# Performance work log

Hardware: AMD Instinct MI355X
Metric: run time of the kernel (lower is better)

## Reference

```python
import jax, jax.numpy as jnp
import numpy as np

NUM_HEADS = 12
EPS = 1e-6


def setup_inputs() -> dict:
    key = jax.random.key(0)
    k1, k2, k3, k4 = jax.random.split(key, 4)
    N, B, D = 1025, 8, 768
    x = jax.random.normal(k1, (N, B, D), dtype=jnp.float32)
    # torch nn.Linear weights: [out_features, in_features]
    w_qkv = jax.random.normal(k2, (3 * D, D), dtype=jnp.float32) * (D ** -0.5)
    w_proj = jax.random.normal(k3, (D, D), dtype=jnp.float32) * (D ** -0.5)
    b_proj = jax.random.normal(k4, (D,), dtype=jnp.float32) * 0.01
    return {"x": x, "w_qkv": w_qkv, "w_proj": w_proj, "b_proj": b_proj}


def reference(x, w_qkv, w_proj, b_proj):
    N, B, D = x.shape
    H = NUM_HEADS
    hd = D // H
    scale = hd ** -0.5
    scale_vv = scale * 1.0  # scale_multiplier = 1.0

    xb = jnp.transpose(x, (1, 0, 2))  # [B, N, D]
    qkv = xb @ w_qkv.T  # [B, N, 3D]
    qkv = qkv.reshape(B, N, 3, H, hd).transpose(2, 0, 3, 1, 4)  # [3, B, H, N, hd]
    q, k, v = qkv[0], qkv[1], qkv[2]

    # QK path: only row 0 of out_ori survives the masking, compute just that row
    scores0 = jnp.einsum('bhqd,bhkd->bhqk', q[:, :, :1], k) * scale  # [B,H,1,N]
    attn0 = jax.nn.softmax(scores0, axis=-1)
    out0 = jnp.einsum('bhqk,bhkd->bhqd', attn0, v)  # [B,H,1,hd]

    # VV cosine path: only rows 1: survive
    vn = v / jnp.maximum(jnp.linalg.norm(v, axis=-1, keepdims=True), EPS)
    scores_vv = jnp.einsum('bhqd,bhkd->bhqk', vn[:, :, 1:], vn) * scale_vv  # [B,H,N-1,N]
    attn_vv = jax.nn.softmax(scores_vv, axis=-1)
    out_vv = jnp.einsum('bhqk,bhkd->bhqd', attn_vv, v)  # [B,H,N-1,hd]

    out = jnp.concatenate([out0, out_vv], axis=2)  # [B,H,N,hd]
    out = out.transpose(0, 2, 1, 3).reshape(B, N, D)
    out = out @ w_proj.T + b_proj
    return jnp.transpose(out, (1, 0, 2))  # [N, B, D]
```

## Files before the change

### kernel.cpp

```cpp
#include <hip/hip_runtime.h>

typedef unsigned short u16;
typedef unsigned int   u32;
typedef __attribute__((ext_vector_type(8))) short short8;
typedef __attribute__((ext_vector_type(4))) float f32x4;

#define AS1 __attribute__((address_space(1)))
#define AS3 __attribute__((address_space(3)))

#define NSEQ  1025
#define BB    8
#define DD    768
#define HH    12
#define MROWS 8200
#define MPAD  8320
#define KPAD  1088

__device__ __forceinline__ void gl2lds16(const void* g, void* l) {
  __builtin_amdgcn_global_load_lds((const AS1 u32*)g, (AS3 u32*)l, 16, 0, 0);
}
__device__ __forceinline__ u16 f2bf(float f) {
  u32 u = __float_as_uint(f);
  return (u16)((u + 0x7FFFu + ((u >> 16) & 1u)) >> 16);
}
__device__ __forceinline__ float bf2f(u16 u) { return __uint_as_float(((u32)u) << 16); }

__global__ __launch_bounds__(256) void prep(const float* __restrict__ x,
                                            const float* __restrict__ wqkv,
                                            const float* __restrict__ wproj,
                                            u16* __restrict__ xb,
                                            u16* __restrict__ wkv,
                                            u16* __restrict__ wpj,
                                            float* __restrict__ q0) {
  __shared__ float red[256];
  const int XB_G  = MPAD * 192;
  const int WKV_G = 1536 * 192;
  const int WPJ_G = 768 * 192;
  int tid = threadIdx.x;
  if (blockIdx.x >= 7968) {
    int bid = blockIdx.x - 7968;
    int b = bid / HH, c = bid - b * HH;
    int dp = (c << 6) + (tid >> 2), part = tid & 3;
    const float4* x4 = (const float4*)(x + (size_t)b * DD + part * 192);
    const float4* w4 = (const float4*)(wqkv + (size_t)dp * DD + part * 192);
    float acc = 0.f;
#pragma unroll 4
    for (int e = 0; e < 48; ++e) {
      float4 a = x4[e], w = w4[e];
      acc += a.x * w.x + a.y * w.y + a.z * w.z + a.w * w.w;
    }
    red[tid] = acc;
    __syncthreads();
    if (part == 0) q0[b * DD + dp] = red[tid] + red[tid + 1] + red[tid + 2] + red[tid + 3];
    return;
  }
  int g = blockIdx.x * 256 + tid;
  float4 v;
  u16* dst;
  size_t di;
  if (g < XB_G) {
    int m = g / 192, e4 = g - m * 192;
    if (m < MROWS) {
      int bb = m / NSEQ, ns = m - bb * NSEQ;
      v = ((const float4*)x)[(size_t)(ns * BB + bb) * 192 + e4];
    } else {
      v.x = v.y = v.z = v.w = 0.f;
    }
    dst = xb; di = (size_t)g;
  } else if (g < XB_G + WKV_G) {
    int r = g - XB_G;
    v = ((const float4*)wqkv)[(size_t)147456 + r];
    dst = wkv; di = (size_t)r;
  } else {
    int r = g - XB_G - WKV_G;
    v = ((const float4*)wproj)[r];
    dst = wpj; di = (size_t)r;
  }
  uint2 o;
  o.x = (u32)f2bf(v.x) | ((u32)f2bf(v.y) << 16);
  o.y = (u32)f2bf(v.z) | ((u32)f2bf(v.w) << 16);
  ((uint2*)dst)[di] = o;
}

template <int MODE, int NT>
__global__ __launch_bounds__(256) void gemm_bt(const u16* __restrict__ A,
                                               const u16* __restrict__ W,
                                               u16* __restrict__ Cbf,
                                               float* __restrict__ Cf,
                                               const float* __restrict__ bias,
                                               int ldc) {
  __shared__ u16 sA[128 * 64];
  __shared__ u16 sW[128 * 64];
  const int id = blockIdx.x;
  const int rx = id & 7, qx = id >> 3;
  const int kq = qx / NT;
  const int m_t = rx + (kq << 3);
  if (m_t > 64) return;
  const int n_t = qx - kq * NT;
  const int m0 = m_t << 7, n0 = n_t << 7;

  const int tid = threadIdx.x;
  const int w = tid >> 6, lane = tid & 63;
  const int wm = w & 1, wn = w >> 1;
  const int lc = lane & 15, lr = lane >> 4;

  f32x4 zero4 = {0.f, 0.f, 0.f, 0.f};
  f32x4 acc[4][4];
#pragma unroll
  for (int i = 0; i < 4; ++i)
#pragma unroll
    for (int j = 0; j < 4; ++j) acc[i][j] = zero4;

  const int r0 = tid >> 3;
  const int ko = (tid & 7) << 3;
  const u16* gA = A + (size_t)(m0 + r0) * DD + ko;
  const u16* gW = W + (size_t)(n0 + r0) * DD + ko;
  char* lA = (char*)sA + tid * 16;
  char* lW = (char*)sW + tid * 16;

#pragma unroll 1
  for (int kt = 0; kt < 12; ++kt) {
    __syncthreads();
#pragma unroll
    for (int j = 0; j < 4; ++j) {
      gl2lds16(gA + (size_t)j * 32 * DD + kt * 64, lA + j * 4096);
      gl2lds16(gW + (size_t)j * 32 * DD + kt * 64, lW + j * 4096);
    }
    __syncthreads();
#pragma unroll
    for (int kk = 0; kk < 2; ++kk) {
      short8 af[4], wf[4];
#pragma unroll
      for (int mt = 0; mt < 4; ++mt)
        af[mt] = *(const short8*)((char*)sA + ((wm << 6) + (mt << 4) + lc) * 128 + (kk << 6) + (lr << 4));
#pragma unroll
      for (int nt = 0; nt < 4; ++nt)
        wf[nt] = *(const short8*)((char*)sW + ((wn << 6) + (nt << 4) + lc) * 128 + (kk << 6) + (lr << 4));
#pragma unroll
      for (int mt = 0; mt < 4; ++mt)
#pragma unroll
        for (int nt = 0; nt < 4; ++nt)
          acc[mt][nt] = __builtin_amdgcn_mfma_f32_16x16x32_bf16(af[mt], wf[nt], acc[mt][nt], 0, 0, 0);
    }
  }

  if (MODE == 0) {
#pragma unroll
    for (int mt = 0; mt < 4; ++mt)
#pragma unroll
      for (int r = 0; r < 4; ++r) {
        int m = m0 + (wm << 6) + (mt << 4) + (lr << 2) + r;
        if (m < MROWS) {
          size_t base = (size_t)m * ldc + n0 + (wn << 6) + lc;
#pragma unroll
          for (int nt = 0; nt < 4; ++nt) Cbf[base + (nt << 4)] = f2bf(acc[mt][nt][r]);
        }
      }
  } else {
    float b4[4];
#pragma unroll
    for (int nt = 0; nt < 4; ++nt) b4[nt] = bias[n0 + (wn << 6) + (nt << 4) + lc];
#pragma unroll
    for (int mt = 0; mt < 4; ++mt)
#pragma unroll
      for (int r = 0; r < 4; ++r) {
        int m = m0 + (wm << 6) + (mt << 4) + (lr << 2) + r;
        if (m < MROWS) {
          int bb = m / NSEQ;
          int ns = m - bb * NSEQ;
          float* o = Cf + (size_t)ns * (BB * DD) + bb * DD + n0 + (wn << 6) + lc;
#pragma unroll
          for (int nt = 0; nt < 4; ++nt) o[nt << 4] = acc[mt][nt][r] + b4[nt];
        }
      }
  }
}

__global__ __launch_bounds__(256) void transpose_v(const u16* __restrict__ kv,
                                                   u16* __restrict__ vT,
                                                   u16* __restrict__ vn) {
  __shared__ u16 tile[64][72];
  __shared__ float red[256];
  __shared__ float sInv[64];
  int bid = blockIdx.x;
  int kc = bid % 17;
  int t2 = bid / 17;
  int h = t2 % HH, b = t2 / HH;
  int tid = threadIdx.x;
  int kl = tid >> 2, dc = (tid & 3) << 4;
  int key = kc * 64 + kl;
  u32 vals[8];
  if (key < NSEQ) {
    const u32* g = (const u32*)(kv + ((size_t)b * NSEQ + key) * 1536 + DD + h * 64 + dc);
#pragma unroll
    for (int i = 0; i < 8; ++i) vals[i] = g[i];
  } else {
#pragma unroll
    for (int i = 0; i < 8; ++i) vals[i] = 0;
  }
  float part = 0.f;
#pragma unroll
  for (int i = 0; i < 8; ++i) {
    float a = bf2f((u16)(vals[i] & 0xFFFF));
    float c = bf2f((u16)(vals[i] >> 16));
    part += a * a + c * c;
    ((u32*)&tile[kl][dc])[i] = vals[i];
  }
  red[tid] = part;
  __syncthreads();
  if ((tid & 3) == 0) {
    float s = red[tid] + red[tid + 1] + red[tid + 2] + red[tid + 3];
    sInv[kl] = (key < NSEQ) ? 1.0f / fmaxf(sqrtf(s), 1e-6f) : 0.0f;
  }
  __syncthreads();
  float iv = sInv[kl];
  u32 ovn[8];
#pragma unroll
  for (int i = 0; i < 8; ++i) {
    float a = bf2f((u16)(vals[i] & 0xFFFF)) * iv;
    float c = bf2f((u16)(vals[i] >> 16)) * iv;
    ovn[i] = (u32)f2bf(a) | ((u32)f2bf(c) << 16);
  }
  u32* on = (u32*)(vn + ((size_t)(b * HH + h) * KPAD + key) * 64 + dc);
#pragma unroll
  for (int i = 0; i < 8; ++i) on[i] = ovn[i];
  int dl = tid >> 2, ks = (tid & 3) << 4;
  u32 ov[8];
#pragma unroll
  for (int i = 0; i < 8; ++i)
    ov[i] = (u32)tile[ks + 2 * i][dl] | ((u32)tile[ks + 2 * i + 1][dl] << 16);
  u16* o = vT + (size_t)(b * HH + h) * 64 * KPAD + (size_t)dl * KPAD + kc * 64 + ks;
#pragma unroll
  for (int i = 0; i < 8; ++i) ((u32*)o)[i] = ov[i];
}

__global__ __launch_bounds__(256) void vv_attn(const u16* __restrict__ vn,
                                               const u16* __restrict__ vT,
                                               u16* __restrict__ attn,
                                               const float* __restrict__ q0,
                                               const u16* __restrict__ kv) {
  __shared__ __align__(16) char smem[51200];
  const int tid = threadIdx.x;
  const int bh = blockIdx.x;
  const int b = bh / HH, h = bh - b * HH;

  if (blockIdx.y == 8) {
    float* sq  = (float*)smem;
    float* sc  = (float*)(smem + 256);
    float* red = (float*)(smem + 4608);
    float (*rpv)[68] = (float(*)[68])(smem + 5632);
    if (tid < 64) sq[tid] = q0[b * DD + h * 64 + tid];
    __syncthreads();
    float mx = -1e30f;
    for (int n = tid; n < NSEQ; n += 256) {
      const u32* kr = (const u32*)(kv + ((size_t)b * NSEQ + n) * 1536 + h * 64);
      float s = 0.f;
#pragma unroll
      for (int i = 0; i < 32; ++i) {
        u32 u = kr[i];
        s += bf2f((u16)(u & 0xFFFF)) * sq[2 * i] + bf2f((u16)(u >> 16)) * sq[2 * i + 1];
      }
      s *= 0.125f;
      sc[n] = s;
      mx = fmaxf(mx, s);
    }
    red[tid] = mx;
    __syncthreads();
    for (int st = 128; st > 0; st >>= 1) {
      if (tid < st) red[tid] = fmaxf(red[tid], red[tid + st]);
      __syncthreads();
    }
    mx = red[0];
    __syncthreads();
    float ds = 0.f;
    for (int n = tid; n < NSEQ; n += 256) {
      float p = __expf(sc[n] - mx);
      sc[n] = p;
      ds += p;
    }
    red[tid] = ds;
    __syncthreads();
    for (int st = 128; st > 0; st >>= 1) {
      if (tid < st) red[tid] += red[tid + st];
      __syncthreads();
    }
    float den = red[0];
    __syncthreads();
    int kp = tid >> 3, dc = (tid & 7) << 3;
    const u16* vb = kv + (size_t)b * NSEQ * 1536 + DD + h * 64 + dc;
    float acc[8];
#pragma unroll
    for (int i = 0; i < 8; ++i) acc[i] = 0.f;
#pragma unroll 4
    for (int j = 0; j < 32; ++j) {
      int n = kp + (j << 5);
      uint4 v = *(const uint4*)(vb + (size_t)n * 1536);
      float p = sc[n];
      acc[0] += p * bf2f((u16)(v.x & 0xFFFF));
      acc[1] += p * bf2f((u16)(v.x >> 16));
      acc[2] += p * bf2f((u16)(v.y & 0xFFFF));
      acc[3] += p * bf2f((u16)(v.y >> 16));
      acc[4] += p * bf2f((u16)(v.z & 0xFFFF));
      acc[5] += p * bf2f((u16)(v.z >> 16));
      acc[6] += p * bf2f((u16)(v.w & 0xFFFF));
      acc[7] += p * bf2f((u16)(v.w >> 16));
    }
    if (kp == 0) {
      uint4 v = *(const uint4*)(vb + (size_t)1024 * 1536);
      float p = sc[1024];
      acc[0] += p * bf2f((u16)(v.x & 0xFFFF));
      acc[1] += p * bf2f((u16)(v.x >> 16));
      acc[2] += p * bf2f((u16)(v.y & 0xFFFF));
      acc[3] += p * bf2f((u16)(v.y >> 16));
      acc[4] += p * bf2f((u16)(v.z & 0xFFFF));
      acc[5] += p * bf2f((u16)(v.z >> 16));
      acc[6] += p * bf2f((u16)(v.w & 0xFFFF));
      acc[7] += p * bf2f((u16)(v.w >> 16));
    }
#pragma unroll
    for (int i = 0; i < 8; ++i) rpv[kp][dc + i] = acc[i];
    __syncthreads();
    if (tid < 64) {
      float s = 0.f;
#pragma unroll
      for (int p = 0; p < 32; ++p) s += rpv[p][tid];
      attn[(size_t)b * NSEQ * DD + h * 64 + tid] = f2bf(s / den);
    }
    return;
  }

  char* cQ = smem;
  char* cK = smem + 16384;
  char* cV = smem + 24576;
  char* cP = smem + 32768;

  const int w = tid >> 6, lane = tid & 63;
  const int lc = lane & 15, lr = lane >> 4;
  const int m0 = blockIdx.y << 7;
  const char* nb = (const char*)(vn + (size_t)bh * KPAD * 64);
  const char* tb = (const char*)(vT + (size_t)bh * 64 * KPAD);

#pragma unroll
  for (int j = 0; j < 4; ++j) {
    int lin = (w << 12) + (j << 10) + (lane << 4);
    int hf = lin >> 13, r = (lin >> 6) & 127, off = lin & 63;
    gl2lds16(nb + (size_t)(1 + m0 + r) * 128 + hf * 64 + off, cQ + lin);
  }

  f32x4 zero4 = {0.f, 0.f, 0.f, 0.f};
  f32x4 oacc[2][4];
  f32x4 dacc[2];
#pragma unroll
  for (int i = 0; i < 2; ++i) {
    dacc[i] = zero4;
#pragma unroll
    for (int j = 0; j < 4; ++j) oacc[i][j] = zero4;
  }
  short8 ones;
#pragma unroll
  for (int i = 0; i < 8; ++i) ones[i] = (short)0x3F80;

#pragma unroll 1
  for (int kt = 0; kt < 17; ++kt) {
    __syncthreads();
#pragma unroll
    for (int j = 0; j < 2; ++j) {
      int lin = (w << 11) + (j << 10) + (lane << 4);
      int hf = lin >> 12, r = (lin >> 6) & 63, off = lin & 63;
      gl2lds16(nb + (size_t)(kt * 64 + r) * 128 + hf * 64 + off, cK + lin);
      gl2lds16(tb + (size_t)r * (KPAD * 2) + kt * 128 + hf * 64 + off, cV + lin);
    }
    __syncthreads();

    f32x4 sacc[4][2];
#pragma unroll
    for (int mt = 0; mt < 4; ++mt)
#pragma unroll
      for (int nt = 0; nt < 2; ++nt) sacc[mt][nt] = zero4;
#pragma unroll
    for (int kk = 0; kk < 2; ++kk) {
      short8 ak[4], bq[2];
#pragma unroll
      for (int mt = 0; mt < 4; ++mt)
        ak[mt] = *(const short8*)(cK + (kk << 12) + ((mt << 4) + lc) * 64 + (lr << 4));
#pragma unroll
      for (int nt = 0; nt < 2; ++nt)
        bq[nt] = *(const short8*)(cQ + (kk << 13) + ((w << 5) + (nt << 4) + lc) * 64 + (lr << 4));
#pragma unroll
      for (int mt = 0; mt < 4; ++mt)
#pragma unroll
        for (int nt = 0; nt < 2; ++nt)
          sacc[mt][nt] = __builtin_amdgcn_mfma_f32_16x16x32_bf16(ak[mt], bq[nt], sacc[mt][nt], 0, 0, 0);
    }

#pragma unroll
    for (int mt = 0; mt < 4; ++mt) {
      int kl0 = (mt << 4) + (lr << 2);
#pragma unroll
      for (int nt = 0; nt < 2; ++nt) {
        int q = (w << 5) + (nt << 4) + lc;
        float c0 = sacc[mt][nt][0], c1 = sacc[mt][nt][1];
        float c2 = sacc[mt][nt][2], c3 = sacc[mt][nt][3];
        float p0 = __builtin_fmaf(c0, __builtin_fmaf(c0, 0.0078125f, 0.125f), 1.0f);
        float p1 = __builtin_fmaf(c1, __builtin_fmaf(c1, 0.0078125f, 0.125f), 1.0f);
        float p2 = __builtin_fmaf(c2, __builtin_fmaf(c2, 0.0078125f, 0.125f), 1.0f);
        float p3 = __builtin_fmaf(c3, __builtin_fmaf(c3, 0.0078125f, 0.125f), 1.0f);
        uint2 pv;
        pv.x = __builtin_amdgcn_perm(__float_as_uint(p1), __float_as_uint(p0), 0x07060302u);
        pv.y = __builtin_amdgcn_perm(__float_as_uint(p3), __float_as_uint(p2), 0x07060302u);
        if (kt == 16) {
          pv.x = (kl0 == 0) ? (pv.x & 0xFFFFu) : 0u;
          pv.y = 0u;
        }
        *(uint2*)(cP + q * 144 + (kl0 << 1)) = pv;
      }
    }

#pragma unroll
    for (int kk = 0; kk < 2; ++kk) {
      short8 ap[2], bv[4];
#pragma unroll
      for (int mt = 0; mt < 2; ++mt)
        ap[mt] = *(const short8*)(cP + ((w << 5) + (mt << 4) + lc) * 144 + (kk << 6) + (lr << 4));
#pragma unroll
      for (int nt = 0; nt < 4; ++nt)
        bv[nt] = *(const short8*)(cV + (kk << 12) + ((nt << 4) + lc) * 64 + (lr << 4));
#pragma unroll
      for (int mt = 0; mt < 2; ++mt) {
#pragma unroll
        for (int nt = 0; nt < 4; ++nt)
          oacc[mt][nt] = __builtin_amdgcn_mfma_f32_16x16x32_bf16(ap[mt], bv[nt], oacc[mt][nt], 0, 0, 0);
        dacc[mt] = __builtin_amdgcn_mfma_f32_16x16x32_bf16(ap[mt], ones, dacc[mt], 0, 0, 0);
      }
    }
  }

#pragma unroll
  for (int mt = 0; mt < 2; ++mt) {
#pragma unroll
    for (int r = 0; r < 4; ++r) {
      int q = (w << 5) + (mt << 4) + (lr << 2) + r;
      int nseq = 1 + m0 + q;
      float rdn = 1.0f / dacc[mt][r];
      size_t obase = ((size_t)b * NSEQ + nseq) * DD + h * 64 + lc;
#pragma unroll
      for (int nt = 0; nt < 4; ++nt) attn[obase + (nt << 4)] = f2bf(oacc[mt][nt][r] * rdn);
    }
  }
}

extern "C" void kernel_launch(void* const* d_in, const int* in_sizes, int n_in,
                              void* d_out, int out_size, void* d_ws, size_t ws_size,
                              hipStream_t stream) {
  const float* x      = (const float*)d_in[0];
  const float* w_qkv  = (const float*)d_in[1];
  const float* w_proj = (const float*)d_in[2];
  const float* b_proj = (const float*)d_in[3];
  float* out = (float*)d_out;
  char* ws = (char*)d_ws;

  u16*   xb   = (u16*)(ws + 0);
  u16*   vT   = (u16*)(ws + 0);
  u16*   wkv  = (u16*)(ws + 13369344);
  u16*   wpj  = (u16*)(ws + 15728640);
  u16*   kvb  = (u16*)(ws + 16908288);
  float* q0   = (float*)(ws + 42467328);
  u16*   attn = (u16*)(ws + 42491904);
  u16*   vn   = (u16*)(ws + 55271424);

  prep<<<8064, 256, 0, stream>>>(x, w_qkv, w_proj, xb, wkv, wpj, q0);
  gemm_bt<0, 12><<<864, 256, 0, stream>>>(xb, wkv, kvb, nullptr, nullptr, 1536);
  transpose_v<<<1632, 256, 0, stream>>>(kvb, vT, vn);
  vv_attn<<<dim3(96, 9), 256, 0, stream>>>(vn, vT, attn, q0, kvb);
  gemm_bt<1, 6><<<432, 256, 0, stream>>>(attn, wpj, nullptr, out, b_proj, 768);
}
```

Baseline: 236.1 us.

## Split row-0 attention into own kernel and hold Q fragments in registers

The row-0 QK softmax path moves out of vv_attn into a separate row0_attn kernel, so vv_attn no longer carries its shared-memory footprint or branch. vv_attn now loads its Q tile into registers once and reuses the LDS space for P, which cuts LDS from 51200 to 33792 bytes. It also sets launch_bounds(256,4) for higher occupancy and shrinks the P row stride from 144 to 136 bytes. The trade-offs are one extra kernel launch, higher register pressure from the persistent Q fragments, and possible LDS bank-conflict changes from the new stride.

Result: slower. 251.3 us (+6.4%).

```diff
diff --git a/kernel.cpp b/kernel.cpp
--- a/kernel.cpp
+++ b/kernel.cpp
@@ -35,7 +35,6 @@
   __shared__ float red[256];
   const int XB_G  = MPAD * 192;
   const int WKV_G = 1536 * 192;
-  const int WPJ_G = 768 * 192;
   int tid = threadIdx.x;
   if (blockIdx.x >= 7968) {
     int bid = blockIdx.x - 7968;
@@ -234,109 +233,108 @@
   for (int i = 0; i < 8; ++i) ((u32*)o)[i] = ov[i];
 }
 
-__global__ __launch_bounds__(256) void vv_attn(const u16* __restrict__ vn,
-                                               const u16* __restrict__ vT,
-                                               u16* __restrict__ attn,
-                                               const float* __restrict__ q0,
-                                               const u16* __restrict__ kv) {
-  __shared__ __align__(16) char smem[51200];
-  const int tid = threadIdx.x;
+__global__ __launch_bounds__(256) void row0_attn(const float* __restrict__ q0,
+                                                 const u16* __restrict__ kv,
+                                                 u16* __restrict__ attn) {
+  __shared__ float sq[64];
+  __shared__ float sc[NSEQ];
+  __shared__ float red[256];
+  __shared__ float rpv[32][68];
+  int bid = blockIdx.x;
+  int b = bid / HH, h = bid - b * HH;
+  int tid = threadIdx.x;
+  if (tid < 64) sq[tid] = q0[b * DD + h * 64 + tid];
+  __syncthreads();
+  float mx = -1e30f;
+  for (int n = tid; n < NSEQ; n += 256) {
+    const u32* kr = (const u32*)(kv + ((size_t)b * NSEQ + n) * 1536 + h * 64);
+    float s = 0.f;
+#pragma unroll
+    for (int i = 0; i < 32; ++i) {
+      u32 u = kr[i];
+      s += bf2f((u16)(u & 0xFFFF)) * sq[2 * i] + bf2f((u16)(u >> 16)) * sq[2 * i + 1];
+    }
+    s *= 0.125f;
+    sc[n] = s;
+    mx = fmaxf(mx, s);
+  }
+  red[tid] = mx;
+  __syncthreads();
+  for (int st = 128; st > 0; st >>= 1) {
+    if (tid < st) red[tid] = fmaxf(red[tid], red[tid + st]);
+    __syncthreads();
+  }
+  mx = red[0];
+  __syncthreads();
+  float ds = 0.f;
+  for (int n = tid; n < NSEQ; n += 256) {
+    float p = __expf(sc[n] - mx);
+    sc[n] = p;
+    ds += p;
+  }
+  red[tid] = ds;
+  __syncthreads();
+  for (int st = 128; st > 0; st >>= 1) {
+    if (tid < st) red[tid] += red[tid + st];
+    __syncthreads();
+  }
+  float den = red[0];
+  __syncthreads();
+  int kp = tid >> 3, dc = (tid & 7) << 3;
+  const u16* vb = kv + (size_t)b * NSEQ * 1536 + DD + h * 64 + dc;
+  float acc[8];
+#pragma unroll
+  for (int i = 0; i < 8; ++i) acc[i] = 0.f;
+#pragma unroll 4
+  for (int j = 0; j < 32; ++j) {
+    int n = kp + (j << 5);
+    uint4 v = *(const uint4*)(vb + (size_t)n * 1536);
+    float p = sc[n];
+    acc[0] += p * bf2f((u16)(v.x & 0xFFFF));
+    acc[1] += p * bf2f((u16)(v.x >> 16));
+    acc[2] += p * bf2f((u16)(v.y & 0xFFFF));
+    acc[3] += p * bf2f((u16)(v.y >> 16));
+    acc[4] += p * bf2f((u16)(v.z & 0xFFFF));
+    acc[5] += p * bf2f((u16)(v.z >> 16));
+    acc[6] += p * bf2f((u16)(v.w & 0xFFFF));
+    acc[7] += p * bf2f((u16)(v.w >> 16));
+  }
+  if (kp == 0) {
+    uint4 v = *(const uint4*)(vb + (size_t)1024 * 1536);
+    float p = sc[1024];
+    acc[0] += p * bf2f((u16)(v.x & 0xFFFF));
+    acc[1] += p * bf2f((u16)(v.x >> 16));
+    acc[2] += p * bf2f((u16)(v.y & 0xFFFF));
+    acc[3] += p * bf2f((u16)(v.y >> 16));
+    acc[4] += p * bf2f((u16)(v.z & 0xFFFF));
+    acc[5] += p * bf2f((u16)(v.z >> 16));
+    acc[6] += p * bf2f((u16)(v.w & 0xFFFF));
+    acc[7] += p * bf2f((u16)(v.w >> 16));
+  }
+#pragma unroll
+  for (int i = 0; i < 8; ++i) rpv[kp][dc + i] = acc[i];
+  __syncthreads();
+  if (tid < 64) {
+    float s = 0.f;
+#pragma unroll
+    for (int p = 0; p < 32; ++p) s += rpv[p][tid];
+    attn[(size_t)b * NSEQ * DD + h * 64 + tid] = f2bf(s / den);
+  }
+}
+
+__global__ __launch_bounds__(256, 4) void vv_attn(const u16* __restrict__ vn,
+                                                  const u16* __restrict__ vT,
+                                                  u16* __restrict__ attn) {
+  __shared__ __align__(16) char smem[33792];
+  char* cP = smem;
+  char* cK = smem + 17408;
+  char* cV = smem + 25600;
+
+  const int tid = threadIdx.x, w = tid >> 6, lane = tid & 63;
+  const int lc = lane & 15, lr = lane >> 4;
   const int bh = blockIdx.x;
+  const int m0 = blockIdx.y << 7;
   const int b = bh / HH, h = bh - b * HH;
-
-  if (blockIdx.y == 8) {
-    float* sq  = (float*)smem;
-    float* sc  = (float*)(smem + 256);
-    float* red = (float*)(smem + 4608);
-    float (*rpv)[68] = (float(*)[68])(smem + 5632);
-    if (tid < 64) sq[tid] = q0[b * DD + h * 64 + tid];
-    __syncthreads();
-    float mx = -1e30f;
-    for (int n = tid; n < NSEQ; n += 256) {
-      const u32* kr = (const u32*)(kv + ((size_t)b * NSEQ + n) * 1536 + h * 64);
-      float s = 0.f;
-#pragma unroll
-      for (int i = 0; i < 32; ++i) {
-        u32 u = kr[i];
-        s += bf2f((u16)(u & 0xFFFF)) * sq[2 * i] + bf2f((u16)(u >> 16)) * sq[2 * i + 1];
-      }
-      s *= 0.125f;
-      sc[n] = s;
-      mx = fmaxf(mx, s);
-    }
-    red[tid] = mx;
-    __syncthreads();
-    for (int st = 128; st > 0; st >>= 1) {
-      if (tid < st) red[tid] = fmaxf(red[tid], red[tid + st]);
-      __syncthreads();
-    }
-    mx = red[0];
-    __syncthreads();
-    float ds = 0.f;
-    for (int n = tid; n < NSEQ; n += 256) {
-      float p = __expf(sc[n] - mx);
-      sc[n] = p;
-      ds += p;
-    }
-    red[tid] = ds;
-    __syncthreads();
-    for (int st = 128; st > 0; st >>= 1) {
-      if (tid < st) red[tid] += red[tid + st];
-      __syncthreads();
-    }
-    float den = red[0];
-    __syncthreads();
-    int kp = tid >> 3, dc = (tid & 7) << 3;
-    const u16* vb = kv + (size_t)b * NSEQ * 1536 + DD + h * 64 + dc;
-    float acc[8];
-#pragma unroll
-    for (int i = 0; i < 8; ++i) acc[i] = 0.f;
-#pragma unroll 4
-    for (int j = 0; j < 32; ++j) {
-      int n = kp + (j << 5);
-      uint4 v = *(const uint4*)(vb + (size_t)n * 1536);
-      float p = sc[n];
-      acc[0] += p * bf2f((u16)(v.x & 0xFFFF));
-      acc[1] += p * bf2f((u16)(v.x >> 16));
-      acc[2] += p * bf2f((u16)(v.y & 0xFFFF));
-      acc[3] += p * bf2f((u16)(v.y >> 16));
-      acc[4] += p * bf2f((u16)(v.z & 0xFFFF));
-      acc[5] += p * bf2f((u16)(v.z >> 16));
-      acc[6] += p * bf2f((u16)(v.w & 0xFFFF));
-      acc[7] += p * bf2f((u16)(v.w >> 16));
-    }
-    if (kp == 0) {
-      uint4 v = *(const uint4*)(vb + (size_t)1024 * 1536);
-      float p = sc[1024];
-      acc[0] += p * bf2f((u16)(v.x & 0xFFFF));
-      acc[1] += p * bf2f((u16)(v.x >> 16));
-      acc[2] += p * bf2f((u16)(v.y & 0xFFFF));
-      acc[3] += p * bf2f((u16)(v.y >> 16));
-      acc[4] += p * bf2f((u16)(v.z & 0xFFFF));
-      acc[5] += p * bf2f((u16)(v.z >> 16));
-      acc[6] += p * bf2f((u16)(v.w & 0xFFFF));
-      acc[7] += p * bf2f((u16)(v.w >> 16));
-    }
-#pragma unroll
-    for (int i = 0; i < 8; ++i) rpv[kp][dc + i] = acc[i];
-    __syncthreads();
-    if (tid < 64) {
-      float s = 0.f;
-#pragma unroll
-      for (int p = 0; p < 32; ++p) s += rpv[p][tid];
-      attn[(size_t)b * NSEQ * DD + h * 64 + tid] = f2bf(s / den);
-    }
-    return;
-  }
-
-  char* cQ = smem;
-  char* cK = smem + 16384;
-  char* cV = smem + 24576;
-  char* cP = smem + 32768;
-
-  const int w = tid >> 6, lane = tid & 63;
-  const int lc = lane & 15, lr = lane >> 4;
-  const int m0 = blockIdx.y << 7;
   const char* nb = (const char*)(vn + (size_t)bh * KPAD * 64);
   const char* tb = (const char*)(vT + (size_t)bh * 64 * KPAD);
 
@@ -344,8 +342,16 @@
   for (int j = 0; j < 4; ++j) {
     int lin = (w << 12) + (j << 10) + (lane << 4);
     int hf = lin >> 13, r = (lin >> 6) & 127, off = lin & 63;
-    gl2lds16(nb + (size_t)(1 + m0 + r) * 128 + hf * 64 + off, cQ + lin);
-  }
+    gl2lds16(nb + (size_t)(1 + m0 + r) * 128 + hf * 64 + off, smem + lin);
+  }
+  __syncthreads();
+  short8 qf[2][2];
+#pragma unroll
+  for (int kk = 0; kk < 2; ++kk)
+#pragma unroll
+    for (int nt = 0; nt < 2; ++nt)
+      qf[kk][nt] = *(const short8*)(smem + (kk << 13) + ((w << 5) + (nt << 4) + lc) * 64 + (lr << 4));
+  __syncthreads();
 
   f32x4 zero4 = {0.f, 0.f, 0.f, 0.f};
   f32x4 oacc[2][4];
@@ -379,18 +385,15 @@
       for (int nt = 0; nt < 2; ++nt) sacc[mt][nt] = zero4;
 #pragma unroll
     for (int kk = 0; kk < 2; ++kk) {
-      short8 ak[4], bq[2];
+      short8 ak[4];
 #pragma unroll
       for (int mt = 0; mt < 4; ++mt)
         ak[mt] = *(const short8*)(cK + (kk << 12) + ((mt << 4) + lc) * 64 + (lr << 4));
 #pragma unroll
-      for (int nt = 0; nt < 2; ++nt)
-        bq[nt] = *(const short8*)(cQ + (kk << 13) + ((w << 5) + (nt << 4) + lc) * 64 + (lr << 4));
-#pragma unroll
       for (int mt = 0; mt < 4; ++mt)
 #pragma unroll
         for (int nt = 0; nt < 2; ++nt)
-          sacc[mt][nt] = __builtin_amdgcn_mfma_f32_16x16x32_bf16(ak[mt], bq[nt], sacc[mt][nt], 0, 0, 0);
+          sacc[mt][nt] = __builtin_amdgcn_mfma_f32_16x16x32_bf16(ak[mt], qf[kk][nt], sacc[mt][nt], 0, 0, 0);
     }
 
 #pragma unroll
@@ -412,7 +415,7 @@
           pv.x = (kl0 == 0) ? (pv.x & 0xFFFFu) : 0u;
           pv.y = 0u;
         }
-        *(uint2*)(cP + q * 144 + (kl0 << 1)) = pv;
+        *(uint2*)(cP + q * 136 + (kl0 << 1)) = pv;
       }
     }
 
@@ -421,7 +424,7 @@
       short8 ap[2], bv[4];
 #pragma unroll
       for (int mt = 0; mt < 2; ++mt)
-        ap[mt] = *(const short8*)(cP + ((w << 5) + (mt << 4) + lc) * 144 + (kk << 6) + (lr << 4));
+        ap[mt] = *(const short8*)(cP + ((w << 5) + (mt << 4) + lc) * 136 + (kk << 6) + (lr << 4));
 #pragma unroll
       for (int nt = 0; nt < 4; ++nt)
         bv[nt] = *(const short8*)(cV + (kk << 12) + ((nt << 4) + lc) * 64 + (lr << 4));
@@ -471,6 +474,7 @@
   prep<<<8064, 256, 0, stream>>>(x, w_qkv, w_proj, xb, wkv, wpj, q0);
   gemm_bt<0, 12><<<864, 256, 0, stream>>>(xb, wkv, kvb, nullptr, nullptr, 1536);
   transpose_v<<<1632, 256, 0, stream>>>(kvb, vT, vn);
-  vv_attn<<<dim3(96, 9), 256, 0, stream>>>(vn, vT, attn, q0, kvb);
+  row0_attn<<<96, 256, 0, stream>>>(q0, kvb, attn);
+  vv_attn<<<dim3(96, 8), 256, 0, stream>>>(vn, vT, attn);
   gemm_bt<1, 6><<<432, 256, 0, stream>>>(attn, wpj, nullptr, out, b_proj, 768);
 }
```
